# Performance work log

Hardware: AMD Instinct MI355X
Metric: run time of the kernel (lower is better)

Reference implementation:

```python
import jax, jax.numpy as jnp
import numpy as np

R = 2            # kernel_radius
N_IN = 64
N_OUT = 128
H, W = 209, 133  # input spatial dims (NHWC)
KH, KW = 4 * R + 1, 2 * R + 1


def hex_indices(radius):
    """Coordinates of hexagon cells inside a (4r+1, 2r+1) grid."""
    moves = np.array([[1, 1], [2, 0], [1, -1], [-1, -1], [-2, 0], [-1, 1]])
    out = [[2 * radius, radius]]
    for il in range(1, radius + 1):
        s = np.array([[2 * radius - 2 * il, radius]])
        cur = moves.repeat(il, axis=0).cumsum(axis=0)
        out.extend((s + cur).tolist())
    return np.array(out, dtype=np.int32)


def make_out_mask(h, w, r):
    out_h, out_w = h - 4 * r, w - 2 * r
    mr = (out_w - 1) // 2  # hex radius of the output mask
    f = np.zeros((mr * 4 + 1, mr * 2 + 1), dtype=np.float32)
    for ind in hex_indices(mr):
        f[tuple(ind)] = 1.0
    i_cut = (mr * 4 + 1 - out_h) // 2
    f = f[i_cut:-i_cut, :]
    return f.reshape(out_h, out_w, 1)


_HEX = hex_indices(R)               # [19, 2]
_N_IND = _HEX.shape[0]
# scatter indices matching MakeVariableIndices ordering:
# for ci in range(N_IN): for co in range(N_OUT): for j in range(n_ind)
_HW = np.tile(_HEX, (N_IN * N_OUT, 1))                       # [19*Nin*Nout, 2]
_CI = np.repeat(np.arange(N_IN), _N_IND * N_OUT)
_CO = np.tile(np.repeat(np.arange(N_OUT), _N_IND), N_IN)
_OUT_MASK = jnp.asarray(make_out_mask(H, W, R))              # [201, 129, 1]


def setup_inputs() -> dict:
    key = jax.random.key(0)
    k1, k2, k3 = jax.random.split(key, 3)
    # glorot-normal-ish scale for the sparse kernel weights
    fan = _N_IND * (N_IN + N_OUT) / 2.0
    sparse_weights = jax.random.normal(k1, (_N_IND * N_IN * N_OUT,), jnp.float32) * np.sqrt(1.0 / fan).astype(np.float32)
    x = jax.random.normal(k2, (16, H, W, N_IN), jnp.float32)
    offset = jax.random.normal(k3, (1, 1, 1, N_OUT), jnp.float32) * 0.1
    return {"x": x, "sparse_weights": sparse_weights, "offset": offset}


def reference(x, sparse_weights, offset):
    # rebuild dense hex-masked kernel [KH, KW, N_IN, N_OUT]
    kernel = jnp.zeros((KH, KW, N_IN, N_OUT), dtype=sparse_weights.dtype)
    kernel = kernel.at[_HW[:, 0], _HW[:, 1], _CI, _CO].set(sparse_weights)
    conv = jax.lax.conv_general_dilated(
        x, kernel, window_strides=(1, 1), padding="VALID",
        dimension_numbers=("NHWC", "HWIO", "NHWC"))
    return jax.nn.elu(conv + offset) * _OUT_MASK
```

## Files before the change

kernel.cpp:

```cpp
#include <hip/hip_runtime.h>
#include <math.h>

#define NB   16
#define HH   209
#define WW   133
#define CIN  64
#define COUT 128
#define OH   201
#define OW   129
#define NTAP 19
#define NW   (NTAP*CIN*COUT)

#define XS_STRIDE 72

typedef __attribute__((ext_vector_type(8))) __bf16 bf16x8;
typedef __attribute__((ext_vector_type(4))) float f32x4;
typedef __attribute__((ext_vector_type(4))) unsigned short us4;

__constant__ int c_dh[NTAP] = {4,3,5,6,5,3,2,1,2,4,6,7,8,7,6,4,2,1,0};
__constant__ int c_dw[NTAP] = {2,3,3,2,1,1,2,3,4,4,4,3,2,1,0,0,0,1,2};

__device__ __forceinline__ unsigned short f2bf(float f) {
  unsigned int u = __builtin_bit_cast(unsigned int, f);
  u += 0x7FFFu + ((u >> 16) & 1u);
  return (unsigned short)(u >> 16);
}

__global__ __launch_bounds__(256) void repack_w(const float* __restrict__ w,
                                                unsigned short* __restrict__ wt) {
  int gid = blockIdx.x * 256 + threadIdx.x;
  int ci = gid & 63;
  int co = (gid >> 6) & 127;
  int k  = gid >> 13;
  wt[gid] = f2bf(w[ci * (COUT * NTAP) + co * NTAP + k]);
}

__global__ __launch_bounds__(256) void conv_hex_mfma(const float* __restrict__ x,
                                                     const unsigned short* __restrict__ wt,
                                                     const float* __restrict__ offs,
                                                     float* __restrict__ out) {
  __shared__ unsigned short xs[80 * XS_STRIDE];

  const int tid  = threadIdx.x;
  const int lane = tid & 63;
  const int wv   = tid >> 6;
  const int l15  = lane & 15;
  const int quad = lane >> 4;
  const int n0   = wv * 32;

  const int bid = blockIdx.x;
  const int oi  = bid % OH;
  const int b   = bid / OH;
  const int par = oi & 1;
  const int na  = 65 - par;

  int ad = oi - 100; ad = ad < 0 ? -ad : ad;
  const int lim = 128 - ad;

  int a_lo_raw = 64 - lim - par;
  int a_lo = a_lo_raw <= 0 ? 0 : (a_lo_raw + 1) >> 1;
  int a_hi = (64 + lim - par) >> 1;
  if (a_hi > na - 1) a_hi = na - 1;

  const int f0 = a_lo >> 4;
  const int f1 = a_hi >> 4;
  const int nf = f1 - f0 + 1;
  const int p0 = f0 * 16;

  float* outb = out + (size_t)(b * OH + oi) * OW * COUT;

  {
    const float4 z = make_float4(0.f, 0.f, 0.f, 0.f);
    const int opar = par ^ 1;
    const int nopp = 65 - opar;
    for (int idx = tid; idx < nopp * 32; idx += 256) {
      int q  = idx >> 5;
      int c4 = idx & 31;
      *(float4*)(outb + (size_t)(opar + 2 * q) * COUT + c4 * 4) = z;
    }
    const int hi_start = p0 + nf * 16;
    const int hi_cnt   = na > hi_start ? na - hi_start : 0;
    const int tot      = (p0 + hi_cnt) * 32;
    for (int idx = tid; idx < tot; idx += 256) {
      int q  = idx >> 5;
      int a  = q < p0 ? q : hi_start + (q - p0);
      int c4 = idx & 31;
      *(float4*)(outb + (size_t)(par + 2 * a) * COUT + c4 * 4) = z;
    }
  }

  f32x4 acc[5][2];
  #pragma unroll
  for (int i = 0; i < 5; ++i) {
    #pragma unroll
    for (int j = 0; j < 2; ++j) acc[i][j] = (f32x4){0.f, 0.f, 0.f, 0.f};
  }

  const float* xb = x + (size_t)b * (HH * WW * CIN);

  for (int k = 0; k < NTAP; ++k) {
    const int dh = c_dh[k];
    const int dw = c_dw[k];

    bf16x8 bfrag[2][2];
    {
      const unsigned short* wb = wt + (size_t)k * CIN * COUT;
      #pragma unroll
      for (int j = 0; j < 2; ++j) {
        const unsigned short* wn = wb + (size_t)(n0 + j * 16 + l15) * CIN + quad * 8;
        bfrag[0][j] = *(const bf16x8*)(wn);
        bfrag[1][j] = *(const bf16x8*)(wn + 32);
      }
    }

    const float* xr = xb + (size_t)(oi + dh) * (WW * CIN);
    #pragma unroll 5
    for (int i = 0; i < nf; ++i) {
      int chunk = tid + i * 256;
      int prel  = chunk >> 4;
      int c4    = chunk & 15;
      int col   = par + 2 * (p0 + prel) + dw;
      if (col > WW - 1) col = WW - 1;
      float4 v = *(const float4*)(xr + (size_t)col * CIN + c4 * 4);
      us4 o;
      o.x = f2bf(v.x); o.y = f2bf(v.y); o.z = f2bf(v.z); o.w = f2bf(v.w);
      *(us4*)(&xs[prel * XS_STRIDE + c4 * 4]) = o;
    }
    __syncthreads();

    #pragma unroll
    for (int ks = 0; ks < 2; ++ks) {
      #pragma unroll
      for (int mf = 0; mf < 5; ++mf) {
        if (mf < nf) {
          bf16x8 afrag = *(const bf16x8*)(&xs[(mf * 16 + l15) * XS_STRIDE + ks * 32 + quad * 8]);
          acc[mf][0] = __builtin_amdgcn_mfma_f32_16x16x32_bf16(afrag, bfrag[ks][0], acc[mf][0], 0, 0, 0);
          acc[mf][1] = __builtin_amdgcn_mfma_f32_16x16x32_bf16(afrag, bfrag[ks][1], acc[mf][1], 0, 0, 0);
        }
      }
    }
    __syncthreads();
  }

  const float off0 = offs[n0 + l15];
  const float off1 = offs[n0 + 16 + l15];
  #pragma unroll
  for (int mf = 0; mf < 5; ++mf) {
    if (mf < nf) {
      #pragma unroll
      for (int r = 0; r < 4; ++r) {
        int a  = (f0 + mf) * 16 + quad * 4 + r;
        int oj = par + 2 * a;
        if (oj <= OW - 1) {
          int adj = oj - 64; adj = adj < 0 ? -adj : adj;
          bool valid = adj <= lim;
          float v0 = acc[mf][0][r] + off0;
          float v1 = acc[mf][1][r] + off1;
          float e0 = v0 > 0.f ? v0 : expm1f(v0);
          float e1 = v1 > 0.f ? v1 : expm1f(v1);
          outb[(size_t)oj * COUT + n0 + l15]      = valid ? e0 : 0.f;
          outb[(size_t)oj * COUT + n0 + 16 + l15] = valid ? e1 : 0.f;
        }
      }
    }
  }
}

extern "C" void kernel_launch(void* const* d_in, const int* in_sizes, int n_in,
                              void* d_out, int out_size, void* d_ws, size_t ws_size,
                              hipStream_t stream) {
  const float* x   = (const float*)d_in[0];
  const float* sw  = (const float*)d_in[1];
  const float* off = (const float*)d_in[2];
  float* out = (float*)d_out;

  unsigned short* wtb = (unsigned short*)d_ws;
  repack_w<<<NW / 256, 256, 0, stream>>>(sw, wtb);
  conv_hex_mfma<<<NB * OH, 256, 0, stream>>>(x, wtb, off, out);
}
```

Measured before the change: 463.1 us.

## Stage each input row once and reuse across hex taps with double buffering

Taps are regrouped by input row (9 rows instead of 19 taps). Each staged row in shared memory now serves every tap on that row through a column shift, which cuts redundant global loads and bf16 conversions. The next row is prefetched into registers and written to a second LDS buffer while the MFMAs run, and the trailing barrier is removed. The cost is more register pressure from the staging array and three sets of weight fragments.

```diff
diff --git a/kernel.cpp b/kernel.cpp
--- a/kernel.cpp
+++ b/kernel.cpp
@@ -11,14 +11,11 @@
 #define NTAP 19
 #define NW   (NTAP*CIN*COUT)
 
-#define XS_STRIDE 72
+#define XS 72
 
 typedef __attribute__((ext_vector_type(8))) __bf16 bf16x8;
 typedef __attribute__((ext_vector_type(4))) float f32x4;
 typedef __attribute__((ext_vector_type(4))) unsigned short us4;
-
-__constant__ int c_dh[NTAP] = {4,3,5,6,5,3,2,1,2,4,6,7,8,7,6,4,2,1,0};
-__constant__ int c_dw[NTAP] = {2,3,3,2,1,1,2,3,4,4,4,3,2,1,0,0,0,1,2};
 
 __device__ __forceinline__ unsigned short f2bf(float f) {
   unsigned int u = __builtin_bit_cast(unsigned int, f);
@@ -39,7 +36,12 @@
                                                      const unsigned short* __restrict__ wt,
                                                      const float* __restrict__ offs,
                                                      float* __restrict__ out) {
-  __shared__ unsigned short xs[80 * XS_STRIDE];
+  constexpr int c_start[9] = {0, 1, 3, 6, 8, 11, 13, 16, 18};
+  constexpr int c_cnt[9]   = {1, 2, 3, 2, 3, 2, 3, 2, 1};
+  constexpr int c_k[19]  = {18, 7,17, 6, 8,16, 1, 5, 0, 9,15, 2, 4, 3,10,14, 11,13, 12};
+  constexpr int c_dw[19] = { 2, 3, 1, 2, 4, 0, 3, 1, 2, 4, 0, 3, 1, 2, 4, 0, 3, 1, 2};
+
+  __shared__ unsigned short xs[2][82 * XS];
 
   const int tid  = threadIdx.x;
   const int lane = tid & 63;
@@ -66,6 +68,8 @@
   const int f1 = a_hi >> 4;
   const int nf = f1 - f0 + 1;
   const int p0 = f0 * 16;
+  const int npos   = nf * 16;
+  const int nchunk = (npos + 2) * 16;
 
   float* outb = out + (size_t)(b * OH + oi) * OW * COUT;
 
@@ -78,7 +82,7 @@
       int c4 = idx & 31;
       *(float4*)(outb + (size_t)(opar + 2 * q) * COUT + c4 * 4) = z;
     }
-    const int hi_start = p0 + nf * 16;
+    const int hi_start = p0 + npos;
     const int hi_cnt   = na > hi_start ? na - hi_start : 0;
     const int tot      = (p0 + hi_cnt) * 32;
     for (int idx = tid; idx < tot; idx += 256) {
@@ -91,55 +95,91 @@
 
   f32x4 acc[5][2];
   #pragma unroll
-  for (int i = 0; i < 5; ++i) {
+  for (int i = 0; i < 5; ++i)
     #pragma unroll
     for (int j = 0; j < 2; ++j) acc[i][j] = (f32x4){0.f, 0.f, 0.f, 0.f};
-  }
 
   const float* xb = x + (size_t)b * (HH * WW * CIN);
 
-  for (int k = 0; k < NTAP; ++k) {
-    const int dh = c_dh[k];
-    const int dw = c_dw[k];
-
-    bf16x8 bfrag[2][2];
+  float4 stg[6];
+  bf16x8 bfrag[3][2][2];
+
+  auto load_stg = [&](int r) {
+    const float* xr = xb + (size_t)(oi + r) * (WW * CIN);
+    const int rpar = (par + r) & 1;
+    #pragma unroll
+    for (int i = 0; i < 6; ++i) {
+      int c = tid + i * 256;
+      if (c < nchunk) {
+        int j  = c >> 4;
+        int c4 = c & 15;
+        int col = rpar + 2 * (p0 + j);
+        if (col > WW - 1) col = WW - 1;
+        stg[i] = *(const float4*)(xr + (size_t)col * CIN + c4 * 4);
+      }
+    }
+  };
+  auto store_stg = [&](int buf) {
+    #pragma unroll
+    for (int i = 0; i < 6; ++i) {
+      int c = tid + i * 256;
+      if (c < nchunk) {
+        int j  = c >> 4;
+        int c4 = c & 15;
+        us4 o;
+        o.x = f2bf(stg[i].x); o.y = f2bf(stg[i].y);
+        o.z = f2bf(stg[i].z); o.w = f2bf(stg[i].w);
+        *(us4*)(&xs[buf][j * XS + c4 * 4]) = o;
+      }
+    }
+  };
+
+  load_stg(0);
+  store_stg(0);
+
+  #pragma unroll
+  for (int r = 0; r < 9; ++r) {
     {
-      const unsigned short* wb = wt + (size_t)k * CIN * COUT;
+      const int st = c_start[r], cnt = c_cnt[r];
       #pragma unroll
-      for (int j = 0; j < 2; ++j) {
-        const unsigned short* wn = wb + (size_t)(n0 + j * 16 + l15) * CIN + quad * 8;
-        bfrag[0][j] = *(const bf16x8*)(wn);
-        bfrag[1][j] = *(const bf16x8*)(wn + 32);
-      }
-    }
-
-    const float* xr = xb + (size_t)(oi + dh) * (WW * CIN);
-    #pragma unroll 5
-    for (int i = 0; i < nf; ++i) {
-      int chunk = tid + i * 256;
-      int prel  = chunk >> 4;
-      int c4    = chunk & 15;
-      int col   = par + 2 * (p0 + prel) + dw;
-      if (col > WW - 1) col = WW - 1;
-      float4 v = *(const float4*)(xr + (size_t)col * CIN + c4 * 4);
-      us4 o;
-      o.x = f2bf(v.x); o.y = f2bf(v.y); o.z = f2bf(v.z); o.w = f2bf(v.w);
-      *(us4*)(&xs[prel * XS_STRIDE + c4 * 4]) = o;
-    }
+      for (int t = 0; t < 3; ++t) {
+        if (t < cnt) {
+          const unsigned short* wb = wt + (size_t)c_k[st + t] * (CIN * COUT);
+          #pragma unroll
+          for (int j = 0; j < 2; ++j) {
+            const unsigned short* wn = wb + (size_t)(n0 + j * 16 + l15) * CIN + quad * 8;
+            bfrag[t][0][j] = *(const bf16x8*)(wn);
+            bfrag[t][1][j] = *(const bf16x8*)(wn + 32);
+          }
+        }
+      }
+    }
+    if (r < 8) load_stg(r + 1);
     __syncthreads();
 
-    #pragma unroll
-    for (int ks = 0; ks < 2; ++ks) {
+    {
+      const int st = c_start[r], cnt = c_cnt[r];
+      const unsigned short* bufp = xs[r & 1];
       #pragma unroll
-      for (int mf = 0; mf < 5; ++mf) {
-        if (mf < nf) {
-          bf16x8 afrag = *(const bf16x8*)(&xs[(mf * 16 + l15) * XS_STRIDE + ks * 32 + quad * 8]);
-          acc[mf][0] = __builtin_amdgcn_mfma_f32_16x16x32_bf16(afrag, bfrag[ks][0], acc[mf][0], 0, 0, 0);
-          acc[mf][1] = __builtin_amdgcn_mfma_f32_16x16x32_bf16(afrag, bfrag[ks][1], acc[mf][1], 0, 0, 0);
+      for (int t = 0; t < 3; ++t) {
+        if (t < cnt) {
+          const int s = (par + c_dw[st + t]) >> 1;
+          #pragma unroll
+          for (int ks = 0; ks < 2; ++ks) {
+            #pragma unroll
+            for (int mf = 0; mf < 5; ++mf) {
+              if (mf < nf) {
+                bf16x8 a = *(const bf16x8*)(&bufp[(mf * 16 + l15 + s) * XS + ks * 32 + quad * 8]);
+                acc[mf][0] = __builtin_amdgcn_mfma_f32_16x16x32_bf16(a, bfrag[t][ks][0], acc[mf][0], 0, 0, 0);
+                acc[mf][1] = __builtin_amdgcn_mfma_f32_16x16x32_bf16(a, bfrag[t][ks][1], acc[mf][1], 0, 0, 0);
+              }
+            }
+          }
         }
       }
     }
-    __syncthreads();
+
+    if (r < 8) store_stg((r + 1) & 1);
   }
 
   const float off0 = offs[n0 + l15];
```

New measurement: 414.9 us. 1.12x faster.
